# Kernel optimization log

Measured on AMD Instinct MI355X. Metric: run time of the kernel, lower is better.

## Reference

```python
import jax, jax.numpy as jnp
import numpy as np

N_NODES = 40000
N_EDGES = 640000
DIM_H = 512
N_HEADS = 8
D_HEAD = DIM_H // N_HEADS


def setup_inputs() -> dict:
    key = jax.random.key(0)
    ks = jax.random.split(key, 8)
    x = jax.random.normal(ks[0], (N_NODES, DIM_H), dtype=jnp.float32)
    edge_index = jax.random.randint(ks[1], (2, N_EDGES), 0, N_NODES, dtype=jnp.int32)
    virt_h = jax.random.normal(ks[2], (1, DIM_H), dtype=jnp.float32)
    virt_edge_index = jnp.zeros((2, 1), dtype=jnp.int32)
    s = 1.0 / np.sqrt(DIM_H)
    Wq = jax.random.normal(ks[3], (DIM_H, DIM_H), dtype=jnp.float32) * s
    Wk = jax.random.normal(ks[4], (DIM_H, DIM_H), dtype=jnp.float32) * s
    Wv = jax.random.normal(ks[5], (DIM_H, DIM_H), dtype=jnp.float32) * s
    bn_gamma = jnp.ones((DIM_H,), dtype=jnp.float32)
    bn_beta = jnp.zeros((DIM_H,), dtype=jnp.float32)
    return {"x": x, "edge_index": edge_index, "virt_h": virt_h,
            "virt_edge_index": virt_edge_index, "Wq": Wq, "Wk": Wk, "Wv": Wv,
            "bn_gamma": bn_gamma, "bn_beta": bn_beta}


def _exphormer_attn(x, edge_index, Wq, Wk, Wv):
    N, D = x.shape
    H, d = N_HEADS, D_HEAD
    Q = (x @ Wq).reshape(N, H, d)
    K = (x @ Wk).reshape(N, H, d)
    V = (x @ Wv).reshape(N, H, d)
    src, dst = edge_index[0], edge_index[1]
    scale = np.float32(1.0 / np.sqrt(d))
    # per-edge, per-head score: sum over head dim of elementwise q*k
    score = jnp.einsum('ehd,ehd->eh', K[src], Q[dst]) * scale  # [E, H]
    score = jnp.exp(jnp.clip(score, -5.0, 5.0))[..., None]     # [E, H, 1]
    msg = V[src] * score                                        # [E, H, d]
    wV = jax.ops.segment_sum(msg, dst, num_segments=N)          # [N, H, d]
    Z = jax.ops.segment_sum(score, dst, num_segments=N)         # [N, H, 1]
    return (wV / (Z + 1e-6)).reshape(N, D)


def reference(x, edge_index, virt_h, virt_edge_index, Wq, Wk, Wv, bn_gamma, bn_beta):
    # virt_h / virt_edge_index unused: use_virt_nodes=False
    h_attn = _exphormer_attn(x, edge_index, Wq, Wk, Wv)
    h = x + h_attn  # dropout p=0 -> identity; residual
    # BatchNorm1d (training-mode batch statistics, biased variance)
    mean = jnp.mean(h, axis=0)
    var = jnp.mean(jnp.square(h - mean), axis=0)
    return (h - mean) * jax.lax.rsqrt(var + 1e-5) * bn_gamma + bn_beta
```

## Files before the change

kernel.cpp:

```cpp
#include <hip/hip_runtime.h>
#include <hip/hip_bf16.h>

#define N_NODES 40000
#define M_PAD   40064
#define N_EDGES 640000
#define DIM_H 512
#define QKV_STRIDE 1536

typedef __attribute__((ext_vector_type(8))) short bf16x8_t;
typedef __attribute__((ext_vector_type(4))) float f32x4_t;
typedef __attribute__((ext_vector_type(8))) unsigned short u16x8_t;

static __device__ __forceinline__ unsigned short f2bf(float f) {
    __hip_bfloat16 h = __float2bfloat16(f);
    return *reinterpret_cast<unsigned short*>(&h);
}
static __device__ __forceinline__ float bf2f(unsigned short u) {
    return __uint_as_float(((unsigned)u) << 16);
}
static __device__ __forceinline__ void gll16(const void* g, void* l) {
    __builtin_amdgcn_global_load_lds(
        (const __attribute__((address_space(1))) unsigned int*)g,
        (__attribute__((address_space(3))) unsigned int*)l, 16, 0, 0);
}

__global__ __launch_bounds__(256)
void cast_x(const float* __restrict__ x, unsigned short* __restrict__ xb)
{
    const size_t i = ((size_t)blockIdx.x * 256 + threadIdx.x) * 8;
    const float4 v0 = *(const float4*)&x[i];
    const float4 v1 = *(const float4*)&x[i + 4];
    u16x8_t o;
    o[0] = f2bf(v0.x); o[1] = f2bf(v0.y); o[2] = f2bf(v0.z); o[3] = f2bf(v0.w);
    o[4] = f2bf(v1.x); o[5] = f2bf(v1.y); o[6] = f2bf(v1.z); o[7] = f2bf(v1.w);
    *(u16x8_t*)&xb[i] = o;
}

__global__ __launch_bounds__(256)
void cast_wt(const float* __restrict__ Wq,
             const float* __restrict__ Wk,
             const float* __restrict__ Wv,
             unsigned short* __restrict__ Wt)
{
    __shared__ float tile[32][33];
    const float* W = (blockIdx.z == 0) ? Wq : (blockIdx.z == 1) ? Wk : Wv;
    unsigned short* Wo = Wt + (size_t)blockIdx.z * 512 * 512;
    const int k0 = blockIdx.x * 32, n0 = blockIdx.y * 32;
    const int tx = threadIdx.x & 31, ty0 = threadIdx.x >> 5;
    #pragma unroll
    for (int p = 0; p < 4; ++p) {
        const int r = ty0 + p * 8;
        tile[r][tx] = W[(size_t)(k0 + r) * 512 + n0 + tx];
    }
    __syncthreads();
    #pragma unroll
    for (int p = 0; p < 4; ++p) {
        const int r = ty0 + p * 8;
        Wo[(size_t)(n0 + r) * 512 + k0 + tx] = f2bf(tile[tx][r]);
    }
}

__global__ __launch_bounds__(256)
void qkv_gemm_mfma(const unsigned short* __restrict__ xb,
                   const unsigned short* __restrict__ Wt,
                   unsigned short* __restrict__ qkv)
{
    __shared__ short Asub[128 * 32];
    __shared__ short Bsub[128 * 32];
    const int n0g = blockIdx.x * 128;
    const int m0  = blockIdx.y * 128;
    const int wsel = n0g >> 9;
    const int nc0  = n0g & 511;
    const int tid = threadIdx.x;
    const int l = tid & 63;
    const int w = tid >> 6;
    const int wr = w >> 1, wc = w & 1;
    const int lr = l & 15;
    const int lk = (l >> 4) * 8;

    const int idx0 = tid, idx1 = 256 + tid;
    const int ar0 = idx0 >> 2, ac0 = (idx0 & 3) * 8;
    const int ar1 = idx1 >> 2, ac1 = (idx1 & 3) * 8;

    const unsigned short* Abase = xb + (size_t)m0 * 512;
    const unsigned short* Bbase = Wt + (size_t)wsel * 262144 + (size_t)nc0 * 512;

    f32x4_t acc[4][4];
    #pragma unroll
    for (int i = 0; i < 4; ++i)
        #pragma unroll
        for (int j = 0; j < 4; ++j)
            acc[i][j] = {0.f, 0.f, 0.f, 0.f};

    for (int k0 = 0; k0 < 512; k0 += 32) {
        gll16(Abase + (size_t)ar0 * 512 + k0 + ac0, &Asub[idx0 * 8]);
        gll16(Abase + (size_t)ar1 * 512 + k0 + ac1, &Asub[idx1 * 8]);
        gll16(Bbase + (size_t)ar0 * 512 + k0 + ac0, &Bsub[idx0 * 8]);
        gll16(Bbase + (size_t)ar1 * 512 + k0 + ac1, &Bsub[idx1 * 8]);
        __syncthreads();
        bf16x8_t a[4], b[4];
        #pragma unroll
        for (int fm = 0; fm < 4; ++fm)
            a[fm] = *(const bf16x8_t*)&Asub[(wr * 64 + fm * 16 + lr) * 32 + lk];
        #pragma unroll
        for (int fn = 0; fn < 4; ++fn)
            b[fn] = *(const bf16x8_t*)&Bsub[(wc * 64 + fn * 16 + lr) * 32 + lk];
        #pragma unroll
        for (int fm = 0; fm < 4; ++fm)
            #pragma unroll
            for (int fn = 0; fn < 4; ++fn)
                acc[fm][fn] = __builtin_amdgcn_mfma_f32_16x16x32_bf16(
                                  a[fm], b[fn], acc[fm][fn], 0, 0, 0);
        __syncthreads();
    }

    #pragma unroll
    for (int fm = 0; fm < 4; ++fm)
        #pragma unroll
        for (int fn = 0; fn < 4; ++fn)
            #pragma unroll
            for (int j = 0; j < 4; ++j) {
                const int row = m0 + wr * 64 + fm * 16 + (l >> 4) * 4 + j;
                const int col = n0g + wc * 64 + fn * 16 + lr;
                qkv[(size_t)row * QKV_STRIDE + col] = f2bf(acc[fm][fn][j]);
            }
}

__global__ __launch_bounds__(256)
void csr_hist(const int* __restrict__ ei, int* __restrict__ counts)
{
    const int e = blockIdx.x * 256 + threadIdx.x;
    atomicAdd(&counts[ei[N_EDGES + e]], 1);
}

__global__ __launch_bounds__(1024)
void csr_scan(const int* __restrict__ counts, int* __restrict__ row_ptr)
{
    __shared__ int part[1024];
    const int t = threadIdx.x;
    const int base = t * 40;
    int s = 0;
    for (int i = 0; i < 40; ++i) {
        const int idx = base + i;
        if (idx < N_NODES) s += counts[idx];
    }
    part[t] = s;
    __syncthreads();
    for (int off = 1; off < 1024; off <<= 1) {
        int v = (t >= off) ? part[t - off] : 0;
        __syncthreads();
        part[t] += v;
        __syncthreads();
    }
    int run = (t == 0) ? 0 : part[t - 1];
    for (int i = 0; i < 40; ++i) {
        const int idx = base + i;
        if (idx < N_NODES) { row_ptr[idx] = run; run += counts[idx]; }
    }
    if (t == 0) row_ptr[N_NODES] = part[1023];
}

__global__ __launch_bounds__(256)
void csr_scatter(const int* __restrict__ ei, const int* __restrict__ row_ptr,
                 int* __restrict__ cursor, unsigned short* __restrict__ col)
{
    const int e = blockIdx.x * 256 + threadIdx.x;
    const int dst = ei[N_EDGES + e];
    const int pos = atomicAdd(&cursor[dst], 1);
    col[row_ptr[dst] + pos] = (unsigned short)ei[e];
}

__global__ __launch_bounds__(256)
void aggregate(const unsigned short* __restrict__ qkv,
               const int* __restrict__ row_ptr,
               const unsigned short* __restrict__ col,
               const float* __restrict__ x,
               float* __restrict__ out)
{
    const int node = blockIdx.x * 4 + (threadIdx.x >> 6);
    const int lane = threadIdx.x & 63;
    const int d0 = lane * 8;

    const u16x8_t q8 = *(const u16x8_t*)(qkv + (size_t)node * QKV_STRIDE + d0);
    float q[8];
    #pragma unroll
    for (int j = 0; j < 8; ++j) q[j] = bf2f(q8[j]);

    float acc[8] = {0.f, 0.f, 0.f, 0.f, 0.f, 0.f, 0.f, 0.f};
    float zsum = 0.f;
    const int start = row_ptr[node];
    const int end   = row_ptr[node + 1];

    int e = start;
    for (; e + 2 <= end; e += 2) {
        const int s0 = __builtin_nontemporal_load(&col[e]);
        const int s1 = __builtin_nontemporal_load(&col[e + 1]);
        const unsigned short* B0 = qkv + (size_t)s0 * QKV_STRIDE + d0;
        const unsigned short* B1 = qkv + (size_t)s1 * QKV_STRIDE + d0;
        const u16x8_t kk0 = *(const u16x8_t*)(B0 + 512);
        const u16x8_t vv0 = *(const u16x8_t*)(B0 + 1024);
        const u16x8_t kk1 = *(const u16x8_t*)(B1 + 512);
        const u16x8_t vv1 = *(const u16x8_t*)(B1 + 1024);
        float p0 = 0.f, p1 = 0.f;
        #pragma unroll
        for (int j = 0; j < 8; ++j) {
            p0 = fmaf(bf2f(kk0[j]), q[j], p0);
            p1 = fmaf(bf2f(kk1[j]), q[j], p1);
        }
        p0 += __shfl_xor(p0, 1, 64); p0 += __shfl_xor(p0, 2, 64); p0 += __shfl_xor(p0, 4, 64);
        p1 += __shfl_xor(p1, 1, 64); p1 += __shfl_xor(p1, 2, 64); p1 += __shfl_xor(p1, 4, 64);
        const float sc0 = __expf(fminf(fmaxf(p0 * 0.125f, -5.f), 5.f));
        const float sc1 = __expf(fminf(fmaxf(p1 * 0.125f, -5.f), 5.f));
        zsum += sc0 + sc1;
        #pragma unroll
        for (int j = 0; j < 8; ++j) {
            acc[j] = fmaf(sc0, bf2f(vv0[j]), acc[j]);
            acc[j] = fmaf(sc1, bf2f(vv1[j]), acc[j]);
        }
    }
    if (e < end) {
        const int s0 = __builtin_nontemporal_load(&col[e]);
        const unsigned short* B0 = qkv + (size_t)s0 * QKV_STRIDE + d0;
        const u16x8_t kk0 = *(const u16x8_t*)(B0 + 512);
        const u16x8_t vv0 = *(const u16x8_t*)(B0 + 1024);
        float p0 = 0.f;
        #pragma unroll
        for (int j = 0; j < 8; ++j) p0 = fmaf(bf2f(kk0[j]), q[j], p0);
        p0 += __shfl_xor(p0, 1, 64); p0 += __shfl_xor(p0, 2, 64); p0 += __shfl_xor(p0, 4, 64);
        const float sc0 = __expf(fminf(fmaxf(p0 * 0.125f, -5.f), 5.f));
        zsum += sc0;
        #pragma unroll
        for (int j = 0; j < 8; ++j) acc[j] = fmaf(sc0, bf2f(vv0[j]), acc[j]);
    }

    const float invz = 1.0f / (zsum + 1e-6f);
    const float* xr = x + (size_t)node * 512 + d0;
    float xv[8];
    #pragma unroll
    for (int j = 0; j < 8; ++j) xv[j] = __builtin_nontemporal_load(xr + j);
    float* orow = out + (size_t)node * 512 + d0;
    #pragma unroll
    for (int j = 0; j < 8; ++j)
        __builtin_nontemporal_store(xv[j] + acc[j] * invz, orow + j);
}

__global__ __launch_bounds__(512)
void stats_pass(const float* __restrict__ hbuf, float* __restrict__ stats)
{
    const int c  = threadIdx.x;
    const int r0 = blockIdx.x * 80;
    float sum = 0.f, sq = 0.f;
    for (int i = 0; i < 80; ++i) {
        const float hv = hbuf[(size_t)(r0 + i) * 512 + c];
        sum += hv; sq += hv * hv;
    }
    atomicAdd(&stats[c], sum);
    atomicAdd(&stats[512 + c], sq);
}

__global__ __launch_bounds__(256)
void bn_norm(float* __restrict__ hbuf,
             const float* __restrict__ stats,
             const float* __restrict__ gamma,
             const float* __restrict__ beta)
{
    const size_t i4 = ((size_t)blockIdx.x * 256 + threadIdx.x) * 4;
    const int c = (int)(i4 & 511);
    const float invN = 1.0f / 40000.0f;
    float4 h = *(float4*)&hbuf[i4];
    float hv[4] = {h.x, h.y, h.z, h.w};
    float o[4];
    #pragma unroll
    for (int j = 0; j < 4; ++j) {
        const float mean = stats[c + j] * invN;
        const float var  = stats[512 + c + j] * invN - mean * mean;
        o[j] = (hv[j] - mean) * rsqrtf(var + 1e-5f) * gamma[c + j] + beta[c + j];
    }
    float4 out = {o[0], o[1], o[2], o[3]};
    *(float4*)&hbuf[i4] = out;
}

extern "C" void kernel_launch(void* const* d_in, const int* in_sizes, int n_in,
                              void* d_out, int out_size, void* d_ws, size_t ws_size,
                              hipStream_t stream)
{
    const float* x     = (const float*)d_in[0];
    const int*   ei    = (const int*)d_in[1];
    const float* Wq    = (const float*)d_in[4];
    const float* Wk    = (const float*)d_in[5];
    const float* Wv    = (const float*)d_in[6];
    const float* gamma = (const float*)d_in[7];
    const float* beta  = (const float*)d_in[8];
    float* out = (float*)d_out;

    char* ws = (char*)d_ws;
    unsigned short* qkv    = (unsigned short*)ws;
    unsigned short* xb     = (unsigned short*)(ws + 123076608);
    unsigned short* Wt     = (unsigned short*)(ws + 164102144);
    int*            counts = (int*)           (ws + 165675008);
    int*            cursor = (int*)           (ws + 165835008);
    int*            row_ptr= (int*)           (ws + 165995008);
    unsigned short* col    = (unsigned short*)(ws + 166155024);
    float*          stats  = (float*)         (ws + 167435056);

    hipMemsetAsync(counts, 0, 160000, stream);
    hipMemsetAsync(cursor, 0, 160000, stream);
    hipMemsetAsync(stats,  0, 4096,   stream);
    hipMemsetAsync(xb + (size_t)N_NODES * 512, 0, (size_t)(M_PAD - N_NODES) * 512 * 2, stream);
    hipMemsetAsync(col + N_EDGES, 0, 32, stream);

    cast_x<<<10000, 256, 0, stream>>>(x, xb);
    cast_wt<<<dim3(16, 16, 3), 256, 0, stream>>>(Wq, Wk, Wv, Wt);
    csr_hist<<<2500, 256, 0, stream>>>(ei, counts);
    csr_scan<<<1, 1024, 0, stream>>>(counts, row_ptr);
    csr_scatter<<<2500, 256, 0, stream>>>(ei, row_ptr, cursor, col);
    qkv_gemm_mfma<<<dim3(12, 313), 256, 0, stream>>>(xb, Wt, qkv);
    aggregate<<<10000, 256, 0, stream>>>(qkv, row_ptr, col, x, out);
    stats_pass<<<500, 512, 0, stream>>>(out, stats);
    bn_norm<<<20000, 256, 0, stream>>>(out, stats, gamma, beta);
}
```

Measured before the change: 518.0 us.

## Split fused edge aggregation into separate score and PV passes

Splits the single aggregate kernel into a score pass, which gathers K rows and writes per-edge per-head scores and per-node Z sums to workspace, and a PV pass, which gathers V rows and accumulates the weighted sum. Each pass now touches only half of each gathered row, which may improve cache locality and lower register pressure. The cost is an extra launch, a second walk over CSR and col, and the write and re-read of a 20 MB score buffer placed over the xb region. It also drops the col padding memset and the nontemporal loads on col.

Result: no change. 514.7 us (-0.6%).

```diff
diff --git a/kernel.cpp b/kernel.cpp
--- a/kernel.cpp
+++ b/kernel.cpp
@@ -171,36 +171,32 @@
 }
 
 __global__ __launch_bounds__(256)
-void aggregate(const unsigned short* __restrict__ qkv,
-               const int* __restrict__ row_ptr,
-               const unsigned short* __restrict__ col,
-               const float* __restrict__ x,
-               float* __restrict__ out)
+void score_pass(const unsigned short* __restrict__ qkv,
+                const int* __restrict__ row_ptr,
+                const unsigned short* __restrict__ col,
+                float* __restrict__ s,
+                float* __restrict__ z)
 {
     const int node = blockIdx.x * 4 + (threadIdx.x >> 6);
     const int lane = threadIdx.x & 63;
     const int d0 = lane * 8;
+    const int g = lane >> 3;
+    const bool wlead = (lane & 7) == 0;
 
     const u16x8_t q8 = *(const u16x8_t*)(qkv + (size_t)node * QKV_STRIDE + d0);
     float q[8];
     #pragma unroll
     for (int j = 0; j < 8; ++j) q[j] = bf2f(q8[j]);
 
-    float acc[8] = {0.f, 0.f, 0.f, 0.f, 0.f, 0.f, 0.f, 0.f};
     float zsum = 0.f;
     const int start = row_ptr[node];
     const int end   = row_ptr[node + 1];
 
     int e = start;
     for (; e + 2 <= end; e += 2) {
-        const int s0 = __builtin_nontemporal_load(&col[e]);
-        const int s1 = __builtin_nontemporal_load(&col[e + 1]);
-        const unsigned short* B0 = qkv + (size_t)s0 * QKV_STRIDE + d0;
-        const unsigned short* B1 = qkv + (size_t)s1 * QKV_STRIDE + d0;
-        const u16x8_t kk0 = *(const u16x8_t*)(B0 + 512);
-        const u16x8_t vv0 = *(const u16x8_t*)(B0 + 1024);
-        const u16x8_t kk1 = *(const u16x8_t*)(B1 + 512);
-        const u16x8_t vv1 = *(const u16x8_t*)(B1 + 1024);
+        const int s0 = col[e], s1 = col[e + 1];
+        const u16x8_t kk0 = *(const u16x8_t*)(qkv + (size_t)s0 * QKV_STRIDE + 512 + d0);
+        const u16x8_t kk1 = *(const u16x8_t*)(qkv + (size_t)s1 * QKV_STRIDE + 512 + d0);
         float p0 = 0.f, p1 = 0.f;
         #pragma unroll
         for (int j = 0; j < 8; ++j) {
@@ -212,6 +208,52 @@
         const float sc0 = __expf(fminf(fmaxf(p0 * 0.125f, -5.f), 5.f));
         const float sc1 = __expf(fminf(fmaxf(p1 * 0.125f, -5.f), 5.f));
         zsum += sc0 + sc1;
+        if (wlead) {
+            s[(size_t)e * 8 + g]       = sc0;
+            s[(size_t)(e + 1) * 8 + g] = sc1;
+        }
+    }
+    if (e < end) {
+        const int s0 = col[e];
+        const u16x8_t kk0 = *(const u16x8_t*)(qkv + (size_t)s0 * QKV_STRIDE + 512 + d0);
+        float p0 = 0.f;
+        #pragma unroll
+        for (int j = 0; j < 8; ++j) p0 = fmaf(bf2f(kk0[j]), q[j], p0);
+        p0 += __shfl_xor(p0, 1, 64); p0 += __shfl_xor(p0, 2, 64); p0 += __shfl_xor(p0, 4, 64);
+        const float sc0 = __expf(fminf(fmaxf(p0 * 0.125f, -5.f), 5.f));
+        zsum += sc0;
+        if (wlead) s[(size_t)e * 8 + g] = sc0;
+    }
+    if (wlead) z[(size_t)node * 8 + g] = zsum;
+}
+
+__global__ __launch_bounds__(256)
+void pv_pass(const unsigned short* __restrict__ qkv,
+             const int* __restrict__ row_ptr,
+             const unsigned short* __restrict__ col,
+             const float* __restrict__ s,
+             const float* __restrict__ z,
+             const float* __restrict__ x,
+             float* __restrict__ out)
+{
+    const int node = blockIdx.x * 4 + (threadIdx.x >> 6);
+    const int lane = threadIdx.x & 63;
+    const int d0 = lane * 8;
+    const int g = lane >> 3;
+
+    const float invz = 1.0f / (z[(size_t)node * 8 + g] + 1e-6f);
+
+    float acc[8] = {0.f, 0.f, 0.f, 0.f, 0.f, 0.f, 0.f, 0.f};
+    const int start = row_ptr[node];
+    const int end   = row_ptr[node + 1];
+
+    int e = start;
+    for (; e + 2 <= end; e += 2) {
+        const int s0 = col[e], s1 = col[e + 1];
+        const float sc0 = s[(size_t)e * 8 + g];
+        const float sc1 = s[(size_t)(e + 1) * 8 + g];
+        const u16x8_t vv0 = *(const u16x8_t*)(qkv + (size_t)s0 * QKV_STRIDE + 1024 + d0);
+        const u16x8_t vv1 = *(const u16x8_t*)(qkv + (size_t)s1 * QKV_STRIDE + 1024 + d0);
         #pragma unroll
         for (int j = 0; j < 8; ++j) {
             acc[j] = fmaf(sc0, bf2f(vv0[j]), acc[j]);
@@ -219,21 +261,13 @@
         }
     }
     if (e < end) {
-        const int s0 = __builtin_nontemporal_load(&col[e]);
-        const unsigned short* B0 = qkv + (size_t)s0 * QKV_STRIDE + d0;
-        const u16x8_t kk0 = *(const u16x8_t*)(B0 + 512);
-        const u16x8_t vv0 = *(const u16x8_t*)(B0 + 1024);
-        float p0 = 0.f;
-        #pragma unroll
-        for (int j = 0; j < 8; ++j) p0 = fmaf(bf2f(kk0[j]), q[j], p0);
-        p0 += __shfl_xor(p0, 1, 64); p0 += __shfl_xor(p0, 2, 64); p0 += __shfl_xor(p0, 4, 64);
-        const float sc0 = __expf(fminf(fmaxf(p0 * 0.125f, -5.f), 5.f));
-        zsum += sc0;
+        const int s0 = col[e];
+        const float sc0 = s[(size_t)e * 8 + g];
+        const u16x8_t vv0 = *(const u16x8_t*)(qkv + (size_t)s0 * QKV_STRIDE + 1024 + d0);
         #pragma unroll
         for (int j = 0; j < 8; ++j) acc[j] = fmaf(sc0, bf2f(vv0[j]), acc[j]);
     }
 
-    const float invz = 1.0f / (zsum + 1e-6f);
     const float* xr = x + (size_t)node * 512 + d0;
     float xv[8];
     #pragma unroll
@@ -302,12 +336,13 @@
     int*            row_ptr= (int*)           (ws + 165995008);
     unsigned short* col    = (unsigned short*)(ws + 166155024);
     float*          stats  = (float*)         (ws + 167435056);
+    float* s = (float*)(ws + 123076608);
+    float* z = (float*)(ws + 123076608 + 24000000);
 
     hipMemsetAsync(counts, 0, 160000, stream);
     hipMemsetAsync(cursor, 0, 160000, stream);
     hipMemsetAsync(stats,  0, 4096,   stream);
     hipMemsetAsync(xb + (size_t)N_NODES * 512, 0, (size_t)(M_PAD - N_NODES) * 512 * 2, stream);
-    hipMemsetAsync(col + N_EDGES, 0, 32, stream);
 
     cast_x<<<10000, 256, 0, stream>>>(x, xb);
     cast_wt<<<dim3(16, 16, 3), 256, 0, stream>>>(Wq, Wk, Wv, Wt);
@@ -315,7 +350,8 @@
     csr_scan<<<1, 1024, 0, stream>>>(counts, row_ptr);
     csr_scatter<<<2500, 256, 0, stream>>>(ei, row_ptr, cursor, col);
     qkv_gemm_mfma<<<dim3(12, 313), 256, 0, stream>>>(xb, Wt, qkv);
-    aggregate<<<10000, 256, 0, stream>>>(qkv, row_ptr, col, x, out);
+    score_pass<<<10000, 256, 0, stream>>>(qkv, row_ptr, col, s, z);
+    pv_pass<<<10000, 256, 0, stream>>>(qkv, row_ptr, col, s, z, x, out);
     stats_pass<<<500, 512, 0, stream>>>(out, stats);
     bn_norm<<<20000, 256, 0, stream>>>(out, stats, gamma, beta);
 }
```
